# Performance work log

Hardware: AMD Instinct MI355X
Metric: run time of the kernel (lower is better)

Reference implementation:

```python
import jax, jax.numpy as jnp
import numpy as np

MU = 0.34
STD = 0.04
PATCH = 32
LOG_NORM_CONST = float(np.log(STD * np.sqrt(2.0 * np.pi)))


def _patch_means(unet_output, patch):
    # unet_output: [B, C, H, W] with B == 1 (original code implicitly requires it).
    B, C, H, W = unet_output.shape
    hp, wp = H // patch, W // patch
    x = unet_output.reshape(B * C, hp, patch, wp, patch)
    # mean over batch*channel and both intra-patch axes -> [hp, wp]
    return x.mean(axis=(0, 2, 4))


def reference(unet_output, transformer_output):
    means = _patch_means(unet_output, PATCH)              # [hp, wp]
    mask = transformer_output[0] >= 0.5                   # [hp, wp]

    # Positive branch: -log(pdf(mean) + 1e-6); original uses .item() -> detached,
    # so stop_gradient reproduces the (lack of) gradient through this branch.
    m_sg = jax.lax.stop_gradient(means)
    logpdf = -0.5 * jnp.square((m_sg - MU) / STD) - LOG_NORM_CONST
    pos_term = -jnp.log(jnp.exp(logpdf) + 1e-6)

    # Negative branch: MSE against zero = mean^2 (differentiable).
    neg_term = jnp.square(means)

    maskf = mask.astype(means.dtype)
    pos_cnt = jnp.sum(maskf)
    neg_cnt = jnp.sum(1.0 - maskf)
    positive_loss = jnp.sum(pos_term * maskf) / pos_cnt
    negative_loss = jnp.sum(neg_term * (1.0 - maskf)) / neg_cnt
    return positive_loss + negative_loss


def setup_inputs() -> dict:
    key = jax.random.key(0)
    k1, k2 = jax.random.split(key)
    unet_output = jax.random.uniform(k1, (1, 1, 8192, 8192), dtype=jnp.float32)
    transformer_output = jax.random.uniform(k2, (1, 256, 256), dtype=jnp.float32)
    return {"unet_output": unet_output, "transformer_output": transformer_output}
```

## Files before the change

kernel.cpp:

```cpp
#include <hip/hip_runtime.h>
#include <math.h>

#define IMG_W 8192
#define PATCH 32
#define NPATCH 65536
#define NBLK   16384

__global__ __launch_bounds__(256) void fused_patch_loss_kernel(
    const float* __restrict__ x, const float* __restrict__ tmask,
    float* __restrict__ p_pos, float* __restrict__ p_neg,
    float* __restrict__ p_cnt)
{
    const int wave  = threadIdx.x >> 6;
    const int lane  = threadIdx.x & 63;
    const int patch = blockIdx.x * 4 + wave;
    const int ph = patch >> 8;
    const int pw = patch & 255;

    const float* base = x + (size_t)(ph * PATCH) * IMG_W + (size_t)(pw * PATCH);
    const int r0 = lane >> 3;
    const int cv = lane & 7;

    float s = 0.0f;
#pragma unroll
    for (int i = 0; i < 4; ++i) {
        const float4 v = *reinterpret_cast<const float4*>(
            base + (size_t)(i * 8 + r0) * IMG_W + cv * 4);
        s += (v.x + v.y) + (v.z + v.w);
    }

#pragma unroll
    for (int off = 32; off >= 1; off >>= 1)
        s += __shfl_down(s, off, 64);

    __shared__ float s_pos[4], s_neg[4], s_cnt[4];
    if (lane == 0) {
        const float m = s * (1.0f / 1024.0f);
        const float t = tmask[patch];
        const float z = (m - 0.34f) * 25.0f;
        const float logpdf = -0.5f * z * z + 2.2999373f;
        const float pterm = -logf(expf(logpdf) + 1e-6f);
        const float nterm = m * m;
        const bool pos = (t >= 0.5f);
        s_pos[wave] = pos ? pterm : 0.0f;
        s_neg[wave] = pos ? 0.0f  : nterm;
        s_cnt[wave] = pos ? 1.0f  : 0.0f;
    }
    __syncthreads();

    if (threadIdx.x == 0) {
        p_pos[blockIdx.x] = (s_pos[0] + s_pos[1]) + (s_pos[2] + s_pos[3]);
        p_neg[blockIdx.x] = (s_neg[0] + s_neg[1]) + (s_neg[2] + s_neg[3]);
        p_cnt[blockIdx.x] = (s_cnt[0] + s_cnt[1]) + (s_cnt[2] + s_cnt[3]);
    }
}

__global__ __launch_bounds__(1024) void finalize_reduce_kernel(
    const float* __restrict__ p_pos, const float* __restrict__ p_neg,
    const float* __restrict__ p_cnt, float* __restrict__ out)
{
    float pos = 0.0f, neg = 0.0f, cnt = 0.0f;
#pragma unroll
    for (int i = threadIdx.x; i < NBLK; i += 1024) {
        pos += p_pos[i];
        neg += p_neg[i];
        cnt += p_cnt[i];
    }

#pragma unroll
    for (int off = 32; off >= 1; off >>= 1) {
        pos += __shfl_down(pos, off, 64);
        neg += __shfl_down(neg, off, 64);
        cnt += __shfl_down(cnt, off, 64);
    }

    __shared__ float sp[16], sn[16], sc[16];
    const int wave = threadIdx.x >> 6;
    const int lane = threadIdx.x & 63;
    if (lane == 0) { sp[wave] = pos; sn[wave] = neg; sc[wave] = cnt; }
    __syncthreads();

    if (threadIdx.x == 0) {
        float P = 0.0f, N = 0.0f, C = 0.0f;
#pragma unroll
        for (int w = 0; w < 16; ++w) { P += sp[w]; N += sn[w]; C += sc[w]; }
        out[0] = P / C + N / ((float)NPATCH - C);
    }
}

extern "C" void kernel_launch(void* const* d_in, const int* in_sizes, int n_in,
                              void* d_out, int out_size, void* d_ws, size_t ws_size,
                              hipStream_t stream)
{
    const float* unet  = (const float*)d_in[0];
    const float* trans = (const float*)d_in[1];
    float* out = (float*)d_out;

    float* p_pos = (float*)d_ws;
    float* p_neg = p_pos + NBLK;
    float* p_cnt = p_neg + NBLK;

    fused_patch_loss_kernel<<<NBLK, 256, 0, stream>>>(unet, trans, p_pos, p_neg, p_cnt);
    finalize_reduce_kernel<<<1, 1024, 0, stream>>>(p_pos, p_neg, p_cnt, out);
}
```

Measured before the change: 349.5 us.

## Process 8-patch horizontal strips per wave with contiguous row loads

Each wave now handles a 256-float-wide strip of one patch row (8 patches) instead of a single patch. Every row load is then a contiguous 1 KB coalesced access, and each lane issues 32 independent float4 loads for more memory-level parallelism. The block count drops eightfold, which shrinks the partial-sum buffer and the finalize kernel. The cost is fewer waves for the GPU to schedule (2048 blocks) and more per-lane registers.

```diff
diff --git a/kernel.cpp b/kernel.cpp
--- a/kernel.cpp
+++ b/kernel.cpp
@@ -4,7 +4,7 @@
 #define IMG_W 8192
 #define PATCH 32
 #define NPATCH 65536
-#define NBLK   16384
+#define NBLK   2048
 
 __global__ __launch_bounds__(256) void fused_patch_loss_kernel(
     const float* __restrict__ x, const float* __restrict__ tmask,
@@ -13,55 +13,70 @@
 {
     const int wave  = threadIdx.x >> 6;
     const int lane  = threadIdx.x & 63;
-    const int patch = blockIdx.x * 4 + wave;
-    const int ph = patch >> 8;
-    const int pw = patch & 255;
+    const int strip = blockIdx.x * 4 + wave;
+    const int ph    = strip >> 5;
+    const int seg   = strip & 31;
 
-    const float* base = x + (size_t)(ph * PATCH) * IMG_W + (size_t)(pw * PATCH);
-    const int r0 = lane >> 3;
-    const int cv = lane & 7;
+    const float* base = x + (size_t)ph * (PATCH * IMG_W)
+                          + (size_t)seg * 256 + (size_t)lane * 4;
 
-    float s = 0.0f;
+    float s0 = 0.0f, s1 = 0.0f, s2 = 0.0f, s3 = 0.0f;
 #pragma unroll
-    for (int i = 0; i < 4; ++i) {
-        const float4 v = *reinterpret_cast<const float4*>(
-            base + (size_t)(i * 8 + r0) * IMG_W + cv * 4);
-        s += (v.x + v.y) + (v.z + v.w);
+    for (int r = 0; r < 32; r += 4) {
+        const float4 v0 = *reinterpret_cast<const float4*>(base + (size_t)(r + 0) * IMG_W);
+        const float4 v1 = *reinterpret_cast<const float4*>(base + (size_t)(r + 1) * IMG_W);
+        const float4 v2 = *reinterpret_cast<const float4*>(base + (size_t)(r + 2) * IMG_W);
+        const float4 v3 = *reinterpret_cast<const float4*>(base + (size_t)(r + 3) * IMG_W);
+        s0 += (v0.x + v0.y) + (v0.z + v0.w);
+        s1 += (v1.x + v1.y) + (v1.z + v1.w);
+        s2 += (v2.x + v2.y) + (v2.z + v2.w);
+        s3 += (v3.x + v3.y) + (v3.z + v3.w);
     }
+    float s = (s0 + s1) + (s2 + s3);
 
-#pragma unroll
-    for (int off = 32; off >= 1; off >>= 1)
-        s += __shfl_down(s, off, 64);
+    s += __shfl_down(s, 4, 64);
+    s += __shfl_down(s, 2, 64);
+    s += __shfl_down(s, 1, 64);
 
-    __shared__ float s_pos[4], s_neg[4], s_cnt[4];
-    if (lane == 0) {
+    float pos = 0.0f, neg = 0.0f, cnt = 0.0f;
+    if ((lane & 7) == 0) {
         const float m = s * (1.0f / 1024.0f);
+        const int patch = ph * 256 + seg * 8 + (lane >> 3);
         const float t = tmask[patch];
         const float z = (m - 0.34f) * 25.0f;
         const float logpdf = -0.5f * z * z + 2.2999373f;
         const float pterm = -logf(expf(logpdf) + 1e-6f);
-        const float nterm = m * m;
-        const bool pos = (t >= 0.5f);
-        s_pos[wave] = pos ? pterm : 0.0f;
-        s_neg[wave] = pos ? 0.0f  : nterm;
-        s_cnt[wave] = pos ? 1.0f  : 0.0f;
+        if (t >= 0.5f) { pos = pterm; cnt = 1.0f; }
+        else           { neg = m * m; }
     }
+    pos += __shfl_down(pos, 32, 64);
+    neg += __shfl_down(neg, 32, 64);
+    cnt += __shfl_down(cnt, 32, 64);
+    pos += __shfl_down(pos, 16, 64);
+    neg += __shfl_down(neg, 16, 64);
+    cnt += __shfl_down(cnt, 16, 64);
+    pos += __shfl_down(pos, 8, 64);
+    neg += __shfl_down(neg, 8, 64);
+    cnt += __shfl_down(cnt, 8, 64);
+
+    __shared__ float sp[4], sn[4], sc[4];
+    if (lane == 0) { sp[wave] = pos; sn[wave] = neg; sc[wave] = cnt; }
     __syncthreads();
 
     if (threadIdx.x == 0) {
-        p_pos[blockIdx.x] = (s_pos[0] + s_pos[1]) + (s_pos[2] + s_pos[3]);
-        p_neg[blockIdx.x] = (s_neg[0] + s_neg[1]) + (s_neg[2] + s_neg[3]);
-        p_cnt[blockIdx.x] = (s_cnt[0] + s_cnt[1]) + (s_cnt[2] + s_cnt[3]);
+        p_pos[blockIdx.x] = (sp[0] + sp[1]) + (sp[2] + sp[3]);
+        p_neg[blockIdx.x] = (sn[0] + sn[1]) + (sn[2] + sn[3]);
+        p_cnt[blockIdx.x] = (sc[0] + sc[1]) + (sc[2] + sc[3]);
     }
 }
 
-__global__ __launch_bounds__(1024) void finalize_reduce_kernel(
+__global__ __launch_bounds__(256) void finalize_reduce_kernel(
     const float* __restrict__ p_pos, const float* __restrict__ p_neg,
     const float* __restrict__ p_cnt, float* __restrict__ out)
 {
     float pos = 0.0f, neg = 0.0f, cnt = 0.0f;
 #pragma unroll
-    for (int i = threadIdx.x; i < NBLK; i += 1024) {
+    for (int i = threadIdx.x; i < NBLK; i += 256) {
         pos += p_pos[i];
         neg += p_neg[i];
         cnt += p_cnt[i];
@@ -74,16 +89,16 @@
         cnt += __shfl_down(cnt, off, 64);
     }
 
-    __shared__ float sp[16], sn[16], sc[16];
+    __shared__ float sp[4], sn[4], sc[4];
     const int wave = threadIdx.x >> 6;
     const int lane = threadIdx.x & 63;
     if (lane == 0) { sp[wave] = pos; sn[wave] = neg; sc[wave] = cnt; }
     __syncthreads();
 
     if (threadIdx.x == 0) {
-        float P = 0.0f, N = 0.0f, C = 0.0f;
-#pragma unroll
-        for (int w = 0; w < 16; ++w) { P += sp[w]; N += sn[w]; C += sc[w]; }
+        const float P = (sp[0] + sp[1]) + (sp[2] + sp[3]);
+        const float N = (sn[0] + sn[1]) + (sn[2] + sn[3]);
+        const float C = (sc[0] + sc[1]) + (sc[2] + sc[3]);
         out[0] = P / C + N / ((float)NPATCH - C);
     }
 }
@@ -101,5 +116,5 @@
     float* p_cnt = p_neg + NBLK;
 
     fused_patch_loss_kernel<<<NBLK, 256, 0, stream>>>(unet, trans, p_pos, p_neg, p_cnt);
-    finalize_reduce_kernel<<<1, 1024, 0, stream>>>(p_pos, p_neg, p_cnt, out);
+    finalize_reduce_kernel<<<1, 256, 0, stream>>>(p_pos, p_neg, p_cnt, out);
 }
```

After: 350.7 us. No clear change (+0.4%).
